# Performance work log

Hardware: AMD Instinct MI355X
Metric: run time of the kernel (lower is better)

## Reference

```python
import jax, jax.numpy as jnp
import numpy as np

N = 50000      # nodes
E = 800000     # edges (avg degree 16)
F_IN = 128
# (d_in, d_out) for the 9 GCNConv layers with width=256, n_layers=3
DIMS = [(128, 128), (128, 192), (192, 256), (256, 256), (256, 256), (256, 256), (256, 192), (192, 128), (128, 1)]
# ReLU after every conv except loop conv i==n_layers-2 (conv idx 4) and the final conv
RELU = [True, True, True, True, False, True, True, True, False]


def setup_inputs() -> dict:
    key = jax.random.key(0)
    ks = jax.random.split(key, 2 + 2 * len(DIMS))
    inp = {
        "x": jax.random.normal(ks[0], (N, F_IN), dtype=jnp.float32),
        "edge_index": jax.random.randint(ks[1], (2, E), 0, N, dtype=jnp.int64),
    }
    for i, (din, dout) in enumerate(DIMS):
        # Glorot-ish init for weights, small random bias (GCNConv has bias=True)
        inp[f"W{i}"] = jax.random.normal(ks[2 + 2 * i], (din, dout), dtype=jnp.float32) / np.float32(np.sqrt(din))
        inp[f"b{i}"] = jax.random.normal(ks[3 + 2 * i], (dout,), dtype=jnp.float32) * 0.01
    return inp


def _gcn_stack(x, src_f, dst_f, norm, Ws, bs):
    h = x
    for i in range(len(Ws)):
        h = h @ Ws[i]                                  # [N, dout] dense transform first (dout <= din mostly)
        msg = h[src_f] * norm[:, None]                 # gather + edge-normalize  [E+N, dout]
        h = jax.ops.segment_sum(msg, dst_f, num_segments=N) + bs[i]
        if RELU[i]:
            h = jax.nn.relu(h)
        # Dropout layers are identity in eval/inference mode.
    return h


def reference(x, edge_index,
              W0, b0, W1, b1, W2, b2, W3, b3, W4, b4, W5, b5, W6, b6, W7, b7, W8, b8):
    src, dst = edge_index[0], edge_index[1]
    loop = jnp.arange(N, dtype=src.dtype)
    # GCNConv default: add self loops, symmetric normalization D^{-1/2}(A+I)D^{-1/2}
    src_f = jnp.concatenate([src, loop])
    dst_f = jnp.concatenate([dst, loop])
    deg = jax.ops.segment_sum(jnp.ones(E + N, dtype=x.dtype), dst_f, num_segments=N)
    dinv = jax.lax.rsqrt(jnp.maximum(deg, 1.0))        # deg >= 1 thanks to self loops
    norm = dinv[src_f] * dinv[dst_f]                   # per-edge coefficient [E+N]
    Ws = [W0, W1, W2, W3, W4, W5, W6, W7, W8]
    bs = [b0, b1, b2, b3, b4, b5, b6, b7, b8]
    return _gcn_stack(x, src_f, dst_f, norm, Ws, bs)   # [N, 1]
```

## Files before the change

### kernel.cpp

```cpp
#include <hip/hip_runtime.h>


#define TPB 256

using bf16x8 = __attribute__((ext_vector_type(8))) __bf16;
using f32x4  = __attribute__((ext_vector_type(4))) float;

__device__ __forceinline__ unsigned bf16rne(float x) {
    unsigned u = __float_as_uint(x);
    return (u + 0x7fffu + ((u >> 16) & 1u)) >> 16;
}

__device__ __forceinline__ void stage16(const unsigned short* g, unsigned short* l) {
#if __has_builtin(__builtin_amdgcn_global_load_lds)
    __builtin_amdgcn_global_load_lds((const __attribute__((address_space(1))) void*)g,
                                     (__attribute__((address_space(3))) void*)l, 16, 0, 0);
#else
    *(uint4*)((char*)l + (threadIdx.x & 63) * 16) = *(const uint4*)g;
#endif
}


__global__ void zero2_kernel(int* a, int* b, int n) {
    int i = blockIdx.x * blockDim.x + threadIdx.x;
    if (i < n) { a[i] = 0; b[i] = 0; }
}

__global__ void count_kernel(const int* __restrict__ dst, int* __restrict__ cnt, int E) {
    int e = blockIdx.x * blockDim.x + threadIdx.x;
    if (e < E) atomicAdd(&cnt[dst[e]], 1);
}

__global__ void dinv_kernel(const int* __restrict__ cnt, float* __restrict__ dinv, int n) {
    int i = blockIdx.x * blockDim.x + threadIdx.x;
    if (i < n) dinv[i] = rsqrtf((float)(cnt[i] + 1));
}

__global__ void scan1_kernel(const int* __restrict__ cnt, int* __restrict__ rowp,
                             int* __restrict__ bsums, int n) {
    __shared__ int sh[TPB];
    int t = threadIdx.x;
    int i = blockIdx.x * TPB + t;
    int v = (i < n) ? (cnt[i] + 1) : 0;
    sh[t] = v;
    __syncthreads();
    for (int off = 1; off < TPB; off <<= 1) {
        int x = (t >= off) ? sh[t - off] : 0;
        __syncthreads();
        sh[t] += x;
        __syncthreads();
    }
    if (i < n) rowp[i] = sh[t] - v;
    if (t == TPB - 1) bsums[blockIdx.x] = sh[t];
}

__global__ void scan2_kernel(int* __restrict__ bsums, int nb) {
    __shared__ int sh[TPB];
    int t = threadIdx.x;
    int v = (t < nb) ? bsums[t] : 0;
    sh[t] = v;
    __syncthreads();
    for (int off = 1; off < TPB; off <<= 1) {
        int x = (t >= off) ? sh[t - off] : 0;
        __syncthreads();
        sh[t] += x;
        __syncthreads();
    }
    if (t < nb) bsums[t] = sh[t] - v;
}

__global__ void scan3_kernel(int* __restrict__ rowp, const int* __restrict__ bsums, int n) {
    int i = blockIdx.x * TPB + threadIdx.x;
    if (i < n) rowp[i] += bsums[blockIdx.x];
}

__global__ void fill_kernel(const int* __restrict__ src, const int* __restrict__ dst,
                            const float* __restrict__ dinv,
                            const int* __restrict__ rowp, int* __restrict__ fill,
                            unsigned* __restrict__ edges, int E) {
    int e = blockIdx.x * blockDim.x + threadIdx.x;
    if (e >= E) return;
    int s = src[e], d = dst[e];
    int pos = rowp[d] + atomicAdd(&fill[d], 1);
    edges[pos] = (unsigned)s | (bf16rne(dinv[s] * dinv[d]) << 16);
}

__global__ void self_kernel(const int* __restrict__ cnt, const int* __restrict__ rowp,
                            const float* __restrict__ dinv, unsigned* __restrict__ edges,
                            int n) {
    int i = blockIdx.x * blockDim.x + threadIdx.x;
    if (i >= n) return;
    float dv = dinv[i];
    edges[rowp[i] + cnt[i]] = (unsigned)i | (bf16rne(dv * dv) << 16);
}


struct WPtrs { const float* p[8]; };

__global__ void wt_all_kernel(WPtrs wp, unsigned short* __restrict__ Wts) {
    const int cum[9] = {0, 16384, 40960, 90112, 155648, 221184, 286720, 335872, 360448};
    const int Ns[8] = {128, 192, 256, 256, 256, 256, 192, 128};
    const int Ks[8] = {128, 128, 192, 256, 256, 256, 256, 192};
    int id = blockIdx.x * blockDim.x + threadIdx.x;
    if (id >= 360448) return;
    int L = 0;
#pragma unroll
    for (int t = 1; t < 8; t++) if (id >= cum[t]) L = t;
    int lid = id - cum[L];
    int N = Ns[L], K = Ks[L];
    int k = lid / N, n = lid - k * N;
    Wts[cum[L] + n * K + k] = (unsigned short)bf16rne(wp.p[L][lid]);
}

__global__ void cvt_bf16_kernel(const float* __restrict__ in, unsigned short* __restrict__ out,
                                int n4) {
    int i = blockIdx.x * blockDim.x + threadIdx.x;
    if (i >= n4) return;
    float4 v = ((const float4*)in)[i];
    uint2 o;
    o.x = bf16rne(v.x) | (bf16rne(v.y) << 16);
    o.y = bf16rne(v.z) | (bf16rne(v.w) << 16);
    ((uint2*)out)[i] = o;
}


__global__ __launch_bounds__(256) void gemm_mfma_kernel(
    const unsigned short* __restrict__ A, const unsigned short* __restrict__ Wt,
    const float* __restrict__ bias, unsigned short* __restrict__ C,
    int M, int K, int Nc, int doBias, int doRelu, int outChunked) {
    __shared__ unsigned short Qb[128 * 64];
    __shared__ unsigned short Pb[128 * 64];
    int tid = threadIdx.x;
    int l = tid & 63, w = tid >> 6;
    int node0 = blockIdx.x * 128, feat0 = blockIdx.y * 128;

    f32x4 acc[4][4];
#pragma unroll
    for (int i = 0; i < 4; i++)
#pragma unroll
        for (int j = 0; j < 4; j++) acc[i][j] = (f32x4){0.f, 0.f, 0.f, 0.f};

    const unsigned short* gQ[4];
    const unsigned short* gP[4];
    unsigned short* lQ[4];
    unsigned short* lP[4];
#pragma unroll
    for (int h = 0; h < 4; h++) {
        int slot = tid + h * 256;
        int r = slot >> 3, q = slot & 7;
        int qg = q ^ (r & 7);
        int nd = node0 + r; if (nd > M - 1) nd = M - 1;
        int ft = feat0 + r; if (ft > Nc - 1) ft = Nc - 1;
        gQ[h] = A + (size_t)nd * K + qg * 8;
        gP[h] = Wt + (size_t)ft * K + qg * 8;
        lQ[h] = Qb + (size_t)(w * 64 + h * 256) * 8;
        lP[h] = Pb + (size_t)(w * 64 + h * 256) * 8;
    }

    int q4 = l >> 4, m16 = l & 15;
    int featHalf = w & 1, nodeHalf = w >> 1;
    int rP0 = featHalf * 64 + m16;
    int rQ0 = nodeHalf * 64 + m16;
    int sw = m16 & 7;

    for (int k0 = 0; k0 < K; k0 += 64) {
        __syncthreads();
#pragma unroll
        for (int h = 0; h < 4; h++) {
            stage16(gQ[h] + k0, lQ[h]);
            stage16(gP[h] + k0, lP[h]);
        }
        __syncthreads();
#pragma unroll
        for (int ko = 0; ko < 2; ko++) {
            bf16x8 pf[4], qf[4];
#pragma unroll
            for (int i = 0; i < 4; i++)
                pf[i] = *(const bf16x8*)(Pb + (rP0 + i * 16) * 64 + ((ko * 4 + q4) ^ sw) * 8);
#pragma unroll
            for (int j = 0; j < 4; j++)
                qf[j] = *(const bf16x8*)(Qb + (rQ0 + j * 16) * 64 + ((ko * 4 + q4) ^ sw) * 8);
#pragma unroll
            for (int i = 0; i < 4; i++)
#pragma unroll
                for (int j = 0; j < 4; j++)
                    acc[i][j] = __builtin_amdgcn_mfma_f32_16x16x32_bf16(pf[i], qf[j],
                                                                        acc[i][j], 0, 0, 0);
        }
    }

#pragma unroll
    for (int i = 0; i < 4; i++) {
        int gf0 = feat0 + featHalf * 64 + i * 16 + q4 * 4;
        if (gf0 >= Nc) continue;
        float4 bv = make_float4(0.f, 0.f, 0.f, 0.f);
        if (doBias) bv = *(const float4*)(bias + gf0);
        size_t cb = outChunked ? ((size_t)(gf0 >> 5) * ((size_t)M * 32) + (gf0 & 31))
                               : (size_t)gf0;
#pragma unroll
        for (int j = 0; j < 4; j++) {
            int gn = node0 + nodeHalf * 64 + j * 16 + m16;
            if (gn >= M) continue;
            f32x4 v = acc[i][j];
            float x0 = v[0] + bv.x, x1 = v[1] + bv.y;
            float x2 = v[2] + bv.z, x3 = v[3] + bv.w;
            if (doRelu) {
                x0 = fmaxf(x0, 0.f); x1 = fmaxf(x1, 0.f);
                x2 = fmaxf(x2, 0.f); x3 = fmaxf(x3, 0.f);
            }
            uint2 o;
            o.x = bf16rne(x0) | (bf16rne(x1) << 16);
            o.y = bf16rne(x2) | (bf16rne(x3) << 16);
            size_t off = outChunked ? (cb + (size_t)gn * 32) : (cb + (size_t)gn * Nc);
            *(uint2*)(C + off) = o;
        }
    }
}

__global__ void gemv128_bf16_kernel(const unsigned short* __restrict__ A,
                                    const float* __restrict__ w,
                                    float* __restrict__ out, int M) {
    int wid = (blockIdx.x * blockDim.x + threadIdx.x) >> 6;
    int lane = threadIdx.x & 63;
    if (wid >= M) return;
    const unsigned short* a = A + (size_t)wid * 128;
    float a0 = __uint_as_float((unsigned)a[lane] << 16);
    float a1 = __uint_as_float((unsigned)a[lane + 64] << 16);
    float s = a0 * w[lane] + a1 * w[lane + 64];
#pragma unroll
    for (int off = 32; off > 0; off >>= 1) s += __shfl_down(s, off);
    if (lane == 0) out[wid] = s;
}


__global__ __launch_bounds__(256) void agg_group_kernel(
    const uint2* __restrict__ in, const int* __restrict__ rowp,
    const int* __restrict__ cnt, const unsigned* __restrict__ edges,
    const float* __restrict__ bias, uint2* __restrict__ out,
    int nchunks, int NG , int n_nodes, int rowVec2,
    int doBias, int doRelu, int outChunked) {
    int xcd = blockIdx.x & 7;
    int slot = blockIdx.x >> 3;
    int chunk, shareIdx, shareCnt;
    if (nchunks == 8) { chunk = xcd; shareIdx = 0; shareCnt = 1; }
    else if (nchunks == 4) { chunk = xcd >> 1; shareIdx = xcd & 1; shareCnt = 2; }
    else {
        chunk = (xcd < 6) ? xcd : (xcd - 6);
        if (chunk < 2) { shareCnt = 2; shareIdx = (xcd < 6) ? 0 : 1; }
        else { shareCnt = 1; shareIdx = 0; }
    }
    int ngPerShare = (NG + shareCnt - 1) / shareCnt;
    if (slot >= ngPerShare) return;
    int ng = shareIdx * ngPerShare + slot;
    if (ng >= NG) return;

    int wave = threadIdx.x >> 6;
    int lane = threadIdx.x & 63;
    int group = lane >> 3, fl = lane & 7;
    int gb = lane & ~7;
    int node = ng * 32 + wave * 8 + group;
    if (node >= n_nodes) return;

    const uint2* slice = in + (size_t)chunk * n_nodes * 8;
    int s0 = rowp[node];
    int c = cnt[node] + 1;

    float ax[4] = {0.f, 0.f, 0.f, 0.f};
    float ay[4] = {0.f, 0.f, 0.f, 0.f};
    float az[4] = {0.f, 0.f, 0.f, 0.f};
    float aw[4] = {0.f, 0.f, 0.f, 0.f};

    unsigned ew = (fl < c) ? edges[s0 + fl] : 0u;
    for (int base = 0; base < c; base += 8) {
        int nidx = base + 8 + fl;
        unsigned ewn = (nidx < c) ? edges[s0 + nidx] : 0u;
        unsigned e[8];
#pragma unroll
        for (int j = 0; j < 8; j++) e[j] = (unsigned)__shfl((int)ew, gb + j);
        uint2 p[8];
#pragma unroll
        for (int j = 0; j < 8; j++) p[j] = slice[(int)(e[j] & 0xffffu) * 8 + fl];
#pragma unroll
        for (int j = 0; j < 8; j++) {
            float wgt = __uint_as_float(e[j] & 0xffff0000u);
            int q = j & 3;
            ax[q] += wgt * __uint_as_float(p[j].x << 16);
            ay[q] += wgt * __uint_as_float(p[j].x & 0xffff0000u);
            az[q] += wgt * __uint_as_float(p[j].y << 16);
            aw[q] += wgt * __uint_as_float(p[j].y & 0xffff0000u);
        }
        ew = ewn;
    }
    float fx = (ax[0] + ax[1]) + (ax[2] + ax[3]);
    float fy = (ay[0] + ay[1]) + (ay[2] + ay[3]);
    float fz = (az[0] + az[1]) + (az[2] + az[3]);
    float fw = (aw[0] + aw[1]) + (aw[2] + aw[3]);

    if (doBias) {
        float4 bb = ((const float4*)bias)[chunk * 8 + fl];
        fx += bb.x; fy += bb.y; fz += bb.z; fw += bb.w;
    }
    if (doRelu) {
        fx = fmaxf(fx, 0.f); fy = fmaxf(fy, 0.f);
        fz = fmaxf(fz, 0.f); fw = fmaxf(fw, 0.f);
    }
    uint2 o;
    o.x = bf16rne(fx) | (bf16rne(fy) << 16);
    o.y = bf16rne(fz) | (bf16rne(fw) << 16);
    size_t oi = outChunked ? ((size_t)chunk * n_nodes * 8 + (size_t)node * 8 + fl)
                           : ((size_t)node * rowVec2 + chunk * 8 + fl);
    out[oi] = o;
}

__global__ void agg1_kernel(const float* __restrict__ in, const int* __restrict__ rowp,
                            const int* __restrict__ cnt, const unsigned* __restrict__ edges,
                            const float* __restrict__ bias, float* __restrict__ out,
                            int n_nodes, int doRelu) {
    int n = blockIdx.x * blockDim.x + threadIdx.x;
    if (n >= n_nodes) return;
    float acc = 0.f;
    int s0 = rowp[n];
    int c = cnt[n] + 1;
    for (int j = 0; j < c; j++) {
        unsigned e = edges[s0 + j];
        acc += __uint_as_float(e & 0xffff0000u) * in[e & 0xffffu];
    }
    acc += bias[0];
    if (doRelu) acc = fmaxf(acc, 0.f);
    out[n] = acc;
}


extern "C" void kernel_launch(void* const* d_in, const int* in_sizes, int n_in,
                              void* d_out, int out_size, void* d_ws, size_t ws_size,
                              hipStream_t stream) {
    const float* x = (const float*)d_in[0];
    const int* ei = (const int*)d_in[1];
    const int Nn = in_sizes[0] / 128;
    const int E = in_sizes[1] / 2;
    const int* src = ei;
    const int* dst = ei + E;

    char* ws = (char*)d_ws;
    size_t off = 0;
    auto alloc = [&](size_t bytes) -> char* {
        char* p = ws + off;
        off = (off + bytes + 255) & ~(size_t)255;
        return p;
    };
    int* cnt = (int*)alloc((size_t)Nn * 4);
    int* fill = (int*)alloc((size_t)Nn * 4);
    int* rowp = (int*)alloc((size_t)Nn * 4);
    int* bsums = (int*)alloc(1024);
    float* dinv = (float*)alloc((size_t)Nn * 4);
    unsigned* edges = (unsigned*)alloc((size_t)(E + Nn) * 4);
    unsigned short* T = (unsigned short*)alloc((size_t)Nn * 256 * 2);
    unsigned short* H = (unsigned short*)alloc((size_t)Nn * 256 * 2);
    unsigned short* Bx = (unsigned short*)alloc((size_t)Nn * 128 * 2);
    float* F = (float*)alloc((size_t)Nn * 4);
    unsigned short* Wts = (unsigned short*)alloc((size_t)400000 * 2);
    (void)ws_size;

    const int dims[9][2] = {{128,128},{128,192},{192,256},{256,256},{256,256},
                            {256,256},{256,192},{192,128},{128,1}};
    unsigned short* Wt[8];
    {
        size_t o = 0;
        for (int i = 0; i < 8; i++) { Wt[i] = Wts + o; o += (size_t)dims[i][0] * dims[i][1]; }
    }

    int nbN = (Nn + TPB - 1) / TPB;
    int nbE = (E + TPB - 1) / TPB;

    zero2_kernel<<<nbN, TPB, 0, stream>>>(cnt, fill, Nn);
    count_kernel<<<nbE, TPB, 0, stream>>>(dst, cnt, E);
    dinv_kernel<<<nbN, TPB, 0, stream>>>(cnt, dinv, Nn);
    scan1_kernel<<<nbN, TPB, 0, stream>>>(cnt, rowp, bsums, Nn);
    scan2_kernel<<<1, TPB, 0, stream>>>(bsums, nbN);
    scan3_kernel<<<nbN, TPB, 0, stream>>>(rowp, bsums, Nn);
    fill_kernel<<<nbE, TPB, 0, stream>>>(src, dst, dinv, rowp, fill, edges, E);
    self_kernel<<<nbN, TPB, 0, stream>>>(cnt, rowp, dinv, edges, Nn);

    WPtrs wp;
    for (int i = 0; i < 8; i++) wp.p[i] = (const float*)d_in[2 + 2 * i];
    wt_all_kernel<<<(360448 + TPB - 1) / TPB, TPB, 0, stream>>>(wp, Wts);
    cvt_bf16_kernel<<<(Nn * 32 + TPB - 1) / TPB, TPB, 0, stream>>>(x, Bx, Nn * 32);

    auto gemm = [&](const unsigned short* A, int i, unsigned short* C, int K, int Nc,
                    int doBias, int doRelu, int outChunked) {
        const float* b = (const float*)d_in[3 + 2 * i];
        dim3 grid((Nn + 127) / 128, (Nc + 127) / 128);
        gemm_mfma_kernel<<<grid, 256, 0, stream>>>(A, Wt[i], b, C, Nn, K, Nc,
                                                   doBias, doRelu, outChunked);
    };
    int NG = (Nn + 31) / 32;
    auto agg = [&](const unsigned short* inb, unsigned short* outb, int w, int i,
                   int doBias, int doRelu, int outChunked) {
        int nch = w / 32;
        int blocksPerXcd = (nch == 4) ? (NG + 1) / 2 : NG;
        const float* b = (const float*)d_in[3 + 2 * i];
        agg_group_kernel<<<blocksPerXcd * 8, 256, 0, stream>>>(
            (const uint2*)inb, rowp, cnt, edges, b, (uint2*)outb,
            nch, NG, Nn, w / 4, doBias, doRelu, outChunked);
    };

    gemm(Bx, 0, T, 128, 128, 0, 0, 1);
    agg(T, H, 128, 0, 1, 1, 1);
    agg(H, T, 128, 1, 0, 0, 0);
    gemm(T, 1, H, 128, 192, 1, 1, 1);
    agg(H, T, 192, 2, 0, 0, 0);
    gemm(T, 2, H, 192, 256, 1, 1, 0);
    gemm(H, 3, T, 256, 256, 0, 0, 1);
    agg(T, H, 256, 3, 1, 1, 0);
    gemm(H, 4, T, 256, 256, 0, 0, 1);
    agg(T, H, 256, 4, 1, 0, 0);
    gemm(H, 5, T, 256, 256, 0, 0, 1);
    agg(T, H, 256, 5, 1, 1, 0);
    gemm(H, 6, T, 256, 192, 0, 0, 1);
    agg(T, H, 192, 6, 1, 1, 0);
    gemm(H, 7, T, 192, 128, 0, 0, 1);
    agg(T, H, 128, 7, 1, 1, 0);
    gemv128_bf16_kernel<<<(Nn + 3) / 4, 256, 0, stream>>>(H, (const float*)d_in[2 + 16],
                                                          F, Nn);
    agg1_kernel<<<nbN, TPB, 0, stream>>>(F, rowp, cnt, edges, (const float*)d_in[3 + 16],
                                         (float*)d_out, Nn, 0);
}
```

Baseline: 688.4 us.

## Sort nodes by degree for balanced aggregation and rebalance XCD chunk mapping

Adds a degree histogram, bin scan and scatter that build a permutation of nodes ordered by in-degree, so each aggregation wave handles nodes of similar degree and loses less time to divergence on uneven neighbour loops. The aggregation kernel now reads permuted row pointers and counts and writes to the original node index. It also replaces the 6-chunk special case with a uniform unit mapping that splits node groups across XCDs by a factor Q, and uses packed float2 accumulators. Several small preprocessing kernels are merged (dinv into scan1, self loops into fill). The permutation adds an indirection and scatters the output writes.

```diff
diff --git a/kernel.cpp b/kernel.cpp
--- a/kernel.cpp
+++ b/kernel.cpp
@@ -5,6 +5,7 @@
 
 using bf16x8 = __attribute__((ext_vector_type(8))) __bf16;
 using f32x4  = __attribute__((ext_vector_type(4))) float;
+using f32x2  = __attribute__((ext_vector_type(2))) float;
 
 __device__ __forceinline__ unsigned bf16rne(float x) {
     unsigned u = __float_as_uint(x);
@@ -21,9 +22,10 @@
 }
 
 
-__global__ void zero2_kernel(int* a, int* b, int n) {
+__global__ void zinit_kernel(int* cnt, int* fill, int* bins, int* binfill, int n) {
     int i = blockIdx.x * blockDim.x + threadIdx.x;
-    if (i < n) { a[i] = 0; b[i] = 0; }
+    if (i < n) { cnt[i] = 0; fill[i] = 0; }
+    if (i < 64) { bins[i] = 0; binfill[i] = 0; }
 }
 
 __global__ void count_kernel(const int* __restrict__ dst, int* __restrict__ cnt, int E) {
@@ -31,17 +33,13 @@
     if (e < E) atomicAdd(&cnt[dst[e]], 1);
 }
 
-__global__ void dinv_kernel(const int* __restrict__ cnt, float* __restrict__ dinv, int n) {
-    int i = blockIdx.x * blockDim.x + threadIdx.x;
-    if (i < n) dinv[i] = rsqrtf((float)(cnt[i] + 1));
-}
-
 __global__ void scan1_kernel(const int* __restrict__ cnt, int* __restrict__ rowp,
-                             int* __restrict__ bsums, int n) {
+                             int* __restrict__ bsums, float* __restrict__ dinv, int n) {
     __shared__ int sh[TPB];
     int t = threadIdx.x;
     int i = blockIdx.x * TPB + t;
     int v = (i < n) ? (cnt[i] + 1) : 0;
+    if (i < n) dinv[i] = rsqrtf((float)v);
     sh[t] = v;
     __syncthreads();
     for (int off = 1; off < TPB; off <<= 1) {
@@ -74,24 +72,57 @@
     if (i < n) rowp[i] += bsums[blockIdx.x];
 }
 
-__global__ void fill_kernel(const int* __restrict__ src, const int* __restrict__ dst,
-                            const float* __restrict__ dinv,
-                            const int* __restrict__ rowp, int* __restrict__ fill,
-                            unsigned* __restrict__ edges, int E) {
-    int e = blockIdx.x * blockDim.x + threadIdx.x;
-    if (e >= E) return;
-    int s = src[e], d = dst[e];
-    int pos = rowp[d] + atomicAdd(&fill[d], 1);
-    edges[pos] = (unsigned)s | (bf16rne(dinv[s] * dinv[d]) << 16);
-}
-
-__global__ void self_kernel(const int* __restrict__ cnt, const int* __restrict__ rowp,
-                            const float* __restrict__ dinv, unsigned* __restrict__ edges,
-                            int n) {
+__global__ void hist_kernel(const int* __restrict__ cnt, int* __restrict__ bins, int n) {
     int i = blockIdx.x * blockDim.x + threadIdx.x;
     if (i >= n) return;
-    float dv = dinv[i];
-    edges[rowp[i] + cnt[i]] = (unsigned)i | (bf16rne(dv * dv) << 16);
+    int d = cnt[i]; if (d > 63) d = 63;
+    atomicAdd(&bins[d], 1);
+}
+
+__global__ void binscan_kernel(const int* __restrict__ bins, int* __restrict__ binoff) {
+    __shared__ int sh[64];
+    int t = threadIdx.x;
+    int v = bins[t];
+    sh[t] = v;
+    __syncthreads();
+    for (int off = 1; off < 64; off <<= 1) {
+        int x = (t >= off) ? sh[t - off] : 0;
+        __syncthreads();
+        sh[t] += x;
+        __syncthreads();
+    }
+    binoff[t] = sh[t] - v;
+}
+
+__global__ void scatter_kernel(const int* __restrict__ cnt, const int* __restrict__ rowp,
+                               const int* __restrict__ binoff, int* __restrict__ binfill,
+                               int* __restrict__ perm, int* __restrict__ prowp,
+                               int* __restrict__ pcnt, int n) {
+    int i = blockIdx.x * blockDim.x + threadIdx.x;
+    if (i >= n) return;
+    int c = cnt[i];
+    int d = c; if (d > 63) d = 63;
+    int pos = binoff[d] + atomicAdd(&binfill[d], 1);
+    perm[pos] = i;
+    prowp[pos] = rowp[i];
+    pcnt[pos] = c;
+}
+
+__global__ void fillself_kernel(const int* __restrict__ src, const int* __restrict__ dst,
+                                const float* __restrict__ dinv,
+                                const int* __restrict__ rowp, int* __restrict__ fill,
+                                const int* __restrict__ cnt,
+                                unsigned* __restrict__ edges, int E, int n) {
+    int id = blockIdx.x * blockDim.x + threadIdx.x;
+    if (id < E) {
+        int s = src[id], d = dst[id];
+        int pos = rowp[d] + atomicAdd(&fill[d], 1);
+        edges[pos] = (unsigned)s | (bf16rne(dinv[s] * dinv[d]) << 16);
+    } else if (id < E + n) {
+        int i = id - E;
+        float dv = dinv[i];
+        edges[rowp[i] + cnt[i]] = (unsigned)i | (bf16rne(dv * dv) << 16);
+    }
 }
 
 
@@ -234,41 +265,37 @@
 
 
 __global__ __launch_bounds__(256) void agg_group_kernel(
-    const uint2* __restrict__ in, const int* __restrict__ rowp,
-    const int* __restrict__ cnt, const unsigned* __restrict__ edges,
+    const uint2* __restrict__ in, const int* __restrict__ prowp,
+    const int* __restrict__ pcnt, const int* __restrict__ perm,
+    const unsigned* __restrict__ edges,
     const float* __restrict__ bias, uint2* __restrict__ out,
-    int nchunks, int NG , int n_nodes, int rowVec2,
+    int Q, int upx, int ngPerUnit, int NG, int n_nodes, int rowVec2,
     int doBias, int doRelu, int outChunked) {
     int xcd = blockIdx.x & 7;
     int slot = blockIdx.x >> 3;
-    int chunk, shareIdx, shareCnt;
-    if (nchunks == 8) { chunk = xcd; shareIdx = 0; shareCnt = 1; }
-    else if (nchunks == 4) { chunk = xcd >> 1; shareIdx = xcd & 1; shareCnt = 2; }
-    else {
-        chunk = (xcd < 6) ? xcd : (xcd - 6);
-        if (chunk < 2) { shareCnt = 2; shareIdx = (xcd < 6) ? 0 : 1; }
-        else { shareCnt = 1; shareIdx = 0; }
-    }
-    int ngPerShare = (NG + shareCnt - 1) / shareCnt;
-    if (slot >= ngPerShare) return;
-    int ng = shareIdx * ngPerShare + slot;
+    int u = slot / ngPerUnit;
+    int ngIdx = slot - u * ngPerUnit;
+    int unit = xcd * upx + u;
+    int chunk = unit / Q;
+    int q = unit - chunk * Q;
+    int ng = ngIdx * Q + q;
     if (ng >= NG) return;
 
     int wave = threadIdx.x >> 6;
     int lane = threadIdx.x & 63;
     int group = lane >> 3, fl = lane & 7;
     int gb = lane & ~7;
-    int node = ng * 32 + wave * 8 + group;
-    if (node >= n_nodes) return;
+    int i = ng * 32 + wave * 8 + group;
+    if (i >= n_nodes) return;
 
     const uint2* slice = in + (size_t)chunk * n_nodes * 8;
-    int s0 = rowp[node];
-    int c = cnt[node] + 1;
-
-    float ax[4] = {0.f, 0.f, 0.f, 0.f};
-    float ay[4] = {0.f, 0.f, 0.f, 0.f};
-    float az[4] = {0.f, 0.f, 0.f, 0.f};
-    float aw[4] = {0.f, 0.f, 0.f, 0.f};
+    int s0 = prowp[i];
+    int c = pcnt[i] + 1;
+    int node = perm[i];
+
+    f32x2 aA[4], aB[4];
+#pragma unroll
+    for (int k = 0; k < 4; k++) { aA[k] = (f32x2){0.f, 0.f}; aB[k] = (f32x2){0.f, 0.f}; }
 
     unsigned ew = (fl < c) ? edges[s0 + fl] : 0u;
     for (int base = 0; base < c; base += 8) {
@@ -283,30 +310,31 @@
 #pragma unroll
         for (int j = 0; j < 8; j++) {
             float wgt = __uint_as_float(e[j] & 0xffff0000u);
-            int q = j & 3;
-            ax[q] += wgt * __uint_as_float(p[j].x << 16);
-            ay[q] += wgt * __uint_as_float(p[j].x & 0xffff0000u);
-            az[q] += wgt * __uint_as_float(p[j].y << 16);
-            aw[q] += wgt * __uint_as_float(p[j].y & 0xffff0000u);
+            int k = j & 3;
+            f32x2 v0 = {__uint_as_float(p[j].x << 16),
+                        __uint_as_float(p[j].x & 0xffff0000u)};
+            f32x2 v1 = {__uint_as_float(p[j].y << 16),
+                        __uint_as_float(p[j].y & 0xffff0000u)};
+            aA[k] += wgt * v0;
+            aB[k] += wgt * v1;
         }
         ew = ewn;
     }
-    float fx = (ax[0] + ax[1]) + (ax[2] + ax[3]);
-    float fy = (ay[0] + ay[1]) + (ay[2] + ay[3]);
-    float fz = (az[0] + az[1]) + (az[2] + az[3]);
-    float fw = (aw[0] + aw[1]) + (aw[2] + aw[3]);
+    f32x2 sA = (aA[0] + aA[1]) + (aA[2] + aA[3]);
+    f32x2 sB = (aB[0] + aB[1]) + (aB[2] + aB[3]);
 
     if (doBias) {
         float4 bb = ((const float4*)bias)[chunk * 8 + fl];
-        fx += bb.x; fy += bb.y; fz += bb.z; fw += bb.w;
+        sA += (f32x2){bb.x, bb.y};
+        sB += (f32x2){bb.z, bb.w};
     }
     if (doRelu) {
-        fx = fmaxf(fx, 0.f); fy = fmaxf(fy, 0.f);
-        fz = fmaxf(fz, 0.f); fw = fmaxf(fw, 0.f);
+        sA[0] = fmaxf(sA[0], 0.f); sA[1] = fmaxf(sA[1], 0.f);
+        sB[0] = fmaxf(sB[0], 0.f); sB[1] = fmaxf(sB[1], 0.f);
     }
     uint2 o;
-    o.x = bf16rne(fx) | (bf16rne(fy) << 16);
-    o.y = bf16rne(fz) | (bf16rne(fw) << 16);
+    o.x = bf16rne(sA[0]) | (bf16rne(sA[1]) << 16);
+    o.y = bf16rne(sB[0]) | (bf16rne(sB[1]) << 16);
     size_t oi = outChunked ? ((size_t)chunk * n_nodes * 8 + (size_t)node * 8 + fl)
                            : ((size_t)node * rowVec2 + chunk * 8 + fl);
     out[oi] = o;
@@ -353,6 +381,12 @@
     int* rowp = (int*)alloc((size_t)Nn * 4);
     int* bsums = (int*)alloc(1024);
     float* dinv = (float*)alloc((size_t)Nn * 4);
+    int* bins = (int*)alloc(256);
+    int* binoff = (int*)alloc(256);
+    int* binfill = (int*)alloc(256);
+    int* perm = (int*)alloc((size_t)Nn * 4);
+    int* prowp = (int*)alloc((size_t)Nn * 4);
+    int* pcnt = (int*)alloc((size_t)Nn * 4);
     unsigned* edges = (unsigned*)alloc((size_t)(E + Nn) * 4);
     unsigned short* T = (unsigned short*)alloc((size_t)Nn * 256 * 2);
     unsigned short* H = (unsigned short*)alloc((size_t)Nn * 256 * 2);
@@ -371,15 +405,19 @@
 
     int nbN = (Nn + TPB - 1) / TPB;
     int nbE = (E + TPB - 1) / TPB;
-
-    zero2_kernel<<<nbN, TPB, 0, stream>>>(cnt, fill, Nn);
+    int nbEN = (E + Nn + TPB - 1) / TPB;
+
+    zinit_kernel<<<nbN, TPB, 0, stream>>>(cnt, fill, bins, binfill, Nn);
     count_kernel<<<nbE, TPB, 0, stream>>>(dst, cnt, E);
-    dinv_kernel<<<nbN, TPB, 0, stream>>>(cnt, dinv, Nn);
-    scan1_kernel<<<nbN, TPB, 0, stream>>>(cnt, rowp, bsums, Nn);
+    scan1_kernel<<<nbN, TPB, 0, stream>>>(cnt, rowp, bsums, dinv, Nn);
     scan2_kernel<<<1, TPB, 0, stream>>>(bsums, nbN);
     scan3_kernel<<<nbN, TPB, 0, stream>>>(rowp, bsums, Nn);
-    fill_kernel<<<nbE, TPB, 0, stream>>>(src, dst, dinv, rowp, fill, edges, E);
-    self_kernel<<<nbN, TPB, 0, stream>>>(cnt, rowp, dinv, edges, Nn);
+    hist_kernel<<<nbN, TPB, 0, stream>>>(cnt, bins, Nn);
+    binscan_kernel<<<1, 64, 0, stream>>>(bins, binoff);
+    scatter_kernel<<<nbN, TPB, 0, stream>>>(cnt, rowp, binoff, binfill,
+                                            perm, prowp, pcnt, Nn);
+    fillself_kernel<<<nbEN, TPB, 0, stream>>>(src, dst, dinv, rowp, fill, cnt,
+                                              edges, E, Nn);
 
     WPtrs wp;
     for (int i = 0; i < 8; i++) wp.p[i] = (const float*)d_in[2 + 2 * i];
@@ -397,11 +435,14 @@
     auto agg = [&](const unsigned short* inb, unsigned short* outb, int w, int i,
                    int doBias, int doRelu, int outChunked) {
         int nch = w / 32;
-        int blocksPerXcd = (nch == 4) ? (NG + 1) / 2 : NG;
+        int Q = (nch == 8) ? 1 : (nch == 6) ? 4 : 2;
+        int upx = nch * Q / 8;
+        int ngPerUnit = (NG + Q - 1) / Q;
+        int blocksPerXcd = upx * ngPerUnit;
         const float* b = (const float*)d_in[3 + 2 * i];
         agg_group_kernel<<<blocksPerXcd * 8, 256, 0, stream>>>(
-            (const uint2*)inb, rowp, cnt, edges, b, (uint2*)outb,
-            nch, NG, Nn, w / 4, doBias, doRelu, outChunked);
+            (const uint2*)inb, prowp, pcnt, perm, edges, b, (uint2*)outb,
+            Q, upx, ngPerUnit, NG, Nn, w / 4, doBias, doRelu, outChunked);
     };
 
     gemm(Bx, 0, T, 128, 128, 0, 0, 1);
```

Result: slower. 931.2 us (+35.3%).
